# Kernel optimization log

Hardware: AMD Instinct MI355X
Metric: run time of the kernel (lower is better)

The kernel has to match this reference:

```python
import jax, jax.numpy as jnp
import numpy as np

B, S = 2048, 512
INPUT_SIZE, OUTPUT_SIZE = 64, 16
KEY_SIZE, VALUE_SIZE = 64, 64
RECALL_SIZE, MEMORY_SIZE, HIDDEN_SIZE = 2, 3, 32


def setup_inputs() -> dict:
    key = jax.random.key(0)
    ks = jax.random.split(key, 15)
    s = 0.05
    def W(k, o, i):
        return jax.random.normal(k, (o, i), jnp.float32) * s
    def b(k, o):
        return jax.random.normal(k, (o,), jnp.float32) * s
    gru_in = INPUT_SIZE + RECALL_SIZE
    return {
        "inputs": jax.random.normal(ks[0], (B, S, INPUT_SIZE), jnp.float32),
        "w_ih": W(ks[1], 3 * HIDDEN_SIZE, gru_in),
        "w_hh": W(ks[2], 3 * HIDDEN_SIZE, HIDDEN_SIZE),
        "b_ih": b(ks[3], 3 * HIDDEN_SIZE),
        "b_hh": b(ks[4], 3 * HIDDEN_SIZE),
        "W_key": W(ks[5], KEY_SIZE, HIDDEN_SIZE),
        "b_key": b(ks[6], KEY_SIZE),
        "W_query": W(ks[7], KEY_SIZE, HIDDEN_SIZE),
        "b_query": b(ks[8], KEY_SIZE),
        "W_value": W(ks[9], VALUE_SIZE, HIDDEN_SIZE),
        "b_value": b(ks[10], VALUE_SIZE),
        "W_recall": W(ks[11], RECALL_SIZE, VALUE_SIZE),
        "b_recall": b(ks[12], RECALL_SIZE),
        "W_out": W(ks[13], OUTPUT_SIZE, HIDDEN_SIZE),
        "b_out": b(ks[14], OUTPUT_SIZE),
    }


def reference(inputs, w_ih, w_hh, b_ih, b_hh, W_key, b_key, W_query, b_query,
              W_value, b_value, W_recall, b_recall, W_out, b_out):
    Bsz, Slen, _ = inputs.shape
    slot_ids = jnp.arange(MEMORY_SIZE)

    def step(carry, xs):
        h, keys, vals, retr = carry
        xt, t = xs
        # GRUCell (PyTorch gate order r, z, n)
        x = jnp.concatenate([xt, retr], axis=1)
        gx = x @ w_ih.T + b_ih
        gh = h @ w_hh.T + b_hh
        xr, xz, xn = jnp.split(gx, 3, axis=1)
        hr, hz, hn = jnp.split(gh, 3, axis=1)
        r = jax.nn.sigmoid(xr + hr)
        z = jax.nn.sigmoid(xz + hz)
        n = jnp.tanh(xn + r * hn)
        h_new = (1.0 - z) * n + z * h
        # flush hidden state exactly at t == memory_size
        h_new = jnp.where(t == MEMORY_SIZE, 0.0, h_new)
        counter = jnp.minimum(t, MEMORY_SIZE)  # slots written before this step
        # read memory (attention over first `counter` slots)
        q = h_new @ W_query.T + b_query                      # (B, K)
        scores = jnp.einsum('bk,bmk->bm', q, keys)           # (B, M)
        mask = slot_ids < counter
        attn = jax.nn.softmax(jnp.where(mask, scores, -1e30), axis=-1)
        read = jnp.einsum('bm,bmv->bv', attn, vals)          # (B, V)
        retr_new = jnp.where(counter > 0, read @ W_recall.T + b_recall, 0.0)
        # write memory (one-hot scatter into slot t, only while t < memory_size)
        k_w = h_new @ W_key.T + b_key
        v_w = h_new @ W_value.T + b_value
        onehot = (slot_ids == t).astype(keys.dtype)          # all-zero once t >= M
        keys = keys + onehot[None, :, None] * k_w[:, None, :]
        vals = vals + onehot[None, :, None] * v_w[:, None, :]
        out = h_new @ W_out.T + b_out
        return (h_new, keys, vals, retr_new), (out, h_new)

    carry0 = (
        jnp.zeros((Bsz, HIDDEN_SIZE), inputs.dtype),
        jnp.zeros((Bsz, MEMORY_SIZE, KEY_SIZE), inputs.dtype),
        jnp.zeros((Bsz, MEMORY_SIZE, VALUE_SIZE), inputs.dtype),
        jnp.zeros((Bsz, RECALL_SIZE), inputs.dtype),
    )
    xs = (jnp.transpose(inputs, (1, 0, 2)), jnp.arange(Slen))
    _, (outs, hids) = jax.lax.scan(step, carry0, xs)
    outputs = jnp.transpose(outs, (1, 0, 2))                 # (B, S, O)
    hiddens = jax.lax.stop_gradient(jnp.transpose(hids, (1, 0, 2)))  # detached
    return (outputs, hiddens)
```

## Files before the change

kernel.cpp:

```cpp
#include <hip/hip_runtime.h>


typedef __attribute__((ext_vector_type(4))) float f32x4;
typedef __attribute__((ext_vector_type(8))) __bf16 bf16x8;

#define NB 2048
#define SL 512
#define NIN 64
#define NH 32
#define NO 16

__device__ __forceinline__ float rcpf_(float x) { return __builtin_amdgcn_rcpf(x); }
__device__ __forceinline__ float sigmoidf_(float x) {
  return rcpf_(1.0f + __expf(-x));
}
__device__ __forceinline__ float tanhf_(float x) {
  return 1.0f - 2.0f * rcpf_(__expf(2.0f * x) + 1.0f);
}
__device__ __forceinline__ f32x4 splat4(float v) {
  f32x4 r; r[0] = v; r[1] = v; r[2] = v; r[3] = v; return r;
}

template <int CTRL>
__device__ __forceinline__ float dpp_add_(float v) {
  int p = __builtin_amdgcn_update_dpp(0, __float_as_int(v), CTRL, 0xF, 0xF, true);
  return v + __int_as_float(p);
}
__device__ __forceinline__ float rowsum16(float v) {
  v = dpp_add_<0x121>(v);
  v = dpp_add_<0x122>(v);
  v = dpp_add_<0x124>(v);
  v = dpp_add_<0x128>(v);
  return v;
}

__device__ __forceinline__ uint32_t cvtpk_(float lo, float hi) {
  uint32_t r;
  asm("v_cvt_pk_bf16_f32 %0, %1, %2" : "=v"(r) : "v"(lo), "v"(hi));
  return r;
}

__device__ __forceinline__ bf16x8 frag4(uint32_t a, uint32_t b, uint32_t c, uint32_t d) {
  union { uint32_t u[4]; bf16x8 v; } x;
  x.u[0] = a; x.u[1] = b; x.u[2] = c; x.u[3] = d;
  return x.v;
}

__device__ __forceinline__ float pick4v(f32x4 v, int w) {
  float a = (w & 2) ? v[2] : v[0];
  float b = (w & 2) ? v[3] : v[1];
  return (w & 1) ? b : a;
}
__device__ __forceinline__ float pick4f(float a0, float a1, float a2, float a3, int w) {
  float a = (w & 2) ? a2 : a0;
  float b = (w & 2) ? a3 : a1;
  return (w & 1) ? b : a;
}

__device__ __forceinline__ bf16x8 ldfrag(const float* __restrict__ W, int indim,
                                         int row, int k0) {
  bf16x8 r;
#pragma unroll
  for (int j = 0; j < 8; ++j) {
    int k = k0 + j;
    float w = (k < indim) ? W[row * indim + k] : 0.0f;
    r[j] = (__bf16)w;
  }
  return r;
}
__device__ __forceinline__ bf16x8 ldfragS(const float* __restrict__ W, int row, int q4) {
  bf16x8 r;
#pragma unroll
  for (int j = 0; j < 8; ++j) {
    int k = 4 * q4 + (j >> 1) + ((j & 1) ? 16 : 0);
    r[j] = (__bf16)W[row * 32 + k];
  }
  return r;
}
__device__ __forceinline__ bf16x8 ldfragT(const float* __restrict__ W, int ncol,
                                          int col, int k0) {
  bf16x8 r;
#pragma unroll
  for (int j = 0; j < 8; ++j) r[j] = (__bf16)W[(k0 + j) * ncol + col];
  return r;
}

#define MFMA(A, B, C) __builtin_amdgcn_mfma_f32_16x16x32_bf16((A), (B), (C), 0, 0, 0)

__global__ __launch_bounds__(256, 1)
void kvmr_kernel(const float* __restrict__ inputs,
                 const float* __restrict__ w_ih,
                 const float* __restrict__ w_hh,
                 const float* __restrict__ b_ih,
                 const float* __restrict__ b_hh,
                 const float* __restrict__ W_key,
                 const float* __restrict__ b_key,
                 const float* __restrict__ W_query,
                 const float* __restrict__ b_query,
                 const float* __restrict__ W_value,
                 const float* __restrict__ b_value,
                 const float* __restrict__ W_recall,
                 const float* __restrict__ b_recall,
                 const float* __restrict__ W_out,
                 const float* __restrict__ b_out,
                 float* __restrict__ out_all) {
  const int tid = threadIdx.x;
  const int l  = tid & 63;
  const int c  = l & 15;
  const int q4 = l >> 4;
  const int w  = tid >> 6;
  const int b0 = blockIdx.x * 16;

  __shared__ __align__(16) uint32_t h_pk[4][16 * 16];
  __shared__ __align__(16) __bf16 kv_pro[4][3][16 * 64];

  bf16x8 Bih[6][2];
  bf16x8 BhhS[6];
#pragma unroll
  for (int g = 0; g < 6; ++g) {
#pragma unroll
    for (int kc = 0; kc < 2; ++kc)
      Bih[g][kc] = ldfrag(w_ih, 66, 16 * g + c, 32 * kc + 8 * q4);
    BhhS[g] = ldfragS(w_hh, 16 * g + c, q4);
  }
  bf16x8 BqS[4], BkS[4], BvS[4];
#pragma unroll
  for (int g = 0; g < 4; ++g) {
    BqS[g] = ldfragS(W_query, 16 * g + c, q4);
    BkS[g] = ldfragS(W_key,   16 * g + c, q4);
    BvS[g] = ldfragS(W_value, 16 * g + c, q4);
  }
  bf16x8 BoS = ldfragS(W_out, c, q4);

  float wih64[6], wih65[6];
#pragma unroll
  for (int g = 0; g < 6; ++g) {
    wih64[g] = w_ih[(16 * g + c) * 66 + 64];
    wih65[g] = w_ih[(16 * g + c) * 66 + 65];
  }
  float wr0f[4], wr1f[4];
#pragma unroll
  for (int g = 0; g < 4; ++g) {
    wr0f[g] = W_recall[16 * g + c];
    wr1f[g] = W_recall[64 + 16 * g + c];
  }

  float bias_rz[4], bias_xn[2], bias_hn[2];
#pragma unroll
  for (int g = 0; g < 4; ++g) bias_rz[g] = b_ih[16 * g + c] + b_hh[16 * g + c];
#pragma unroll
  for (int gg = 0; gg < 2; ++gg) {
    bias_xn[gg] = b_ih[64 + 16 * gg + c];
    bias_hn[gg] = b_hh[64 + 16 * gg + c];
  }
  float bq4[4], bk4[4], bv4[4];
#pragma unroll
  for (int g = 0; g < 4; ++g) {
    bq4[g] = b_query[16 * g + c];
    bk4[g] = b_key[16 * g + c];
    bv4[g] = b_value[16 * g + c];
  }
  float bo1 = b_out[c];
  float br0 = b_recall[0], br1 = b_recall[1];

  float* outW = out_all + (size_t)(b0 + 4 * q4 + w) * SL * NO + c;
  float* hidW = out_all + (size_t)NB * SL * NO + (size_t)(b0 + 4 * q4 + w) * SL * NH + c;

  f32x4 hD0 = splat4(0.0f), hD1 = splat4(0.0f);
  f32x4 keysR[3][4], valsR[3][4];
#pragma unroll
  for (int s = 0; s < 3; ++s)
#pragma unroll
    for (int g = 0; g < 4; ++g) { keysR[s][g] = splat4(0.0f); valsR[s][g] = splat4(0.0f); }

  f32x4 hPartRZ[4], hPartHN[2];
#pragma unroll
  for (int g = 0; g < 4; ++g) hPartRZ[g] = splat4(bias_rz[g]);
#pragma unroll
  for (int gg = 0; gg < 2; ++gg) hPartHN[gg] = splat4(bias_hn[gg]);
  float retr0c[4] = {0.f, 0.f, 0.f, 0.f};
  float retr1c[4] = {0.f, 0.f, 0.f, 0.f};

  const float* xp = inputs + (size_t)(b0 + c) * (SL * NIN) + 8 * q4;
  f32x4 xb[2][4];
#pragma unroll
  for (int p = 0; p < 2; ++p) {
    const float* xq = xp + p * NIN;
    xb[p][0] = *(const f32x4*)(xq + 0);
    xb[p][1] = *(const f32x4*)(xq + 4);
    xb[p][2] = *(const f32x4*)(xq + 32);
    xb[p][3] = *(const f32x4*)(xq + 36);
  }

#pragma unroll
  for (int t = 0; t < 3; ++t) {
    const int pb = t & 1;
    bf16x8 ax0, ax1;
#pragma unroll
    for (int j = 0; j < 4; ++j) {
      ax0[j]     = (__bf16)xb[pb][0][j];
      ax0[4 + j] = (__bf16)xb[pb][1][j];
      ax1[j]     = (__bf16)xb[pb][2][j];
      ax1[4 + j] = (__bf16)xb[pb][3][j];
    }
    {
      const float* xq = xp + (t + 2) * NIN;
      xb[pb][0] = *(const f32x4*)(xq + 0);
      xb[pb][1] = *(const f32x4*)(xq + 4);
      xb[pb][2] = *(const f32x4*)(xq + 32);
      xb[pb][3] = *(const f32x4*)(xq + 36);
    }

    f32x4 accRZ[4], accXN[2];
#pragma unroll
    for (int g = 0; g < 4; ++g) {
      f32x4 a = hPartRZ[g];
#pragma unroll
      for (int r = 0; r < 4; ++r) a[r] += retr0c[r] * wih64[g] + retr1c[r] * wih65[g];
      a = MFMA(ax0, Bih[g][0], a);
      a = MFMA(ax1, Bih[g][1], a);
      accRZ[g] = a;
    }
#pragma unroll
    for (int gg = 0; gg < 2; ++gg) {
      f32x4 a = splat4(bias_xn[gg]);
#pragma unroll
      for (int r = 0; r < 4; ++r) a[r] += retr0c[r] * wih64[4 + gg] + retr1c[r] * wih65[4 + gg];
      a = MFMA(ax0, Bih[4 + gg][0], a);
      a = MFMA(ax1, Bih[4 + gg][1], a);
      accXN[gg] = a;
    }

    f32x4 hn0, hn1;
#pragma unroll
    for (int r = 0; r < 4; ++r) {
      float rg0 = sigmoidf_(accRZ[0][r]);
      float zg0 = sigmoidf_(accRZ[2][r]);
      float ng0 = tanhf_(accXN[0][r] + rg0 * hPartHN[0][r]);
      hn0[r] = (1.0f - zg0) * ng0 + zg0 * hD0[r];
      float rg1 = sigmoidf_(accRZ[1][r]);
      float zg1 = sigmoidf_(accRZ[3][r]);
      float ng1 = tanhf_(accXN[1][r] + rg1 * hPartHN[1][r]);
      hn1[r] = (1.0f - zg1) * ng1 + zg1 * hD1[r];
    }
    hD0 = hn0; hD1 = hn1;

    hidW[t * NH]      = pick4v(hn0, w);
    hidW[t * NH + 16] = pick4v(hn1, w);
#pragma unroll
    for (int r = 0; r < 4; ++r)
      h_pk[w][(4 * q4 + r) * 16 + c] = cvtpk_(hn0[r], hn1[r]);
    bf16x8 hA = *(const bf16x8*)&h_pk[w][c * 16 + 4 * q4];

#pragma unroll
    for (int g = 0; g < 4; ++g) hPartRZ[g] = MFMA(hA, BhhS[g], splat4(bias_rz[g]));
#pragma unroll
    for (int gg = 0; gg < 2; ++gg) hPartHN[gg] = MFMA(hA, BhhS[4 + gg], splat4(bias_hn[gg]));
    f32x4 oT = MFMA(hA, BoS, splat4(bo1));
    outW[t * NO] = pick4v(oT, w);

    f32x4 qT[4], kT[4], vT[4];
#pragma unroll
    for (int g = 0; g < 4; ++g) {
      qT[g] = MFMA(hA, BqS[g], splat4(bq4[g]));
      kT[g] = MFMA(hA, BkS[g], splat4(bk4[g]));
      vT[g] = MFMA(hA, BvS[g], splat4(bv4[g]));
    }

#pragma unroll
    for (int r = 0; r < 4; ++r) {
      float d0 = qT[0][r] * keysR[0][0][r] + qT[1][r] * keysR[0][1][r] +
                 qT[2][r] * keysR[0][2][r] + qT[3][r] * keysR[0][3][r];
      float d1 = qT[0][r] * keysR[1][0][r] + qT[1][r] * keysR[1][1][r] +
                 qT[2][r] * keysR[1][2][r] + qT[3][r] * keysR[1][3][r];
      float s0 = (t > 0) ? rowsum16(d0) : -1e30f;
      float s1 = (t > 1) ? rowsum16(d1) : -1e30f;
      float s2 = -1e30f;
      float mx = fmaxf(s0, fmaxf(s1, s2));
      float e0 = __expf(s0 - mx), e1 = __expf(s1 - mx), e2 = __expf(s2 - mx);
      float inv = rcpf_(e0 + e1 + e2);
      float u0 = 0.f, u1 = 0.f;
#pragma unroll
      for (int g = 0; g < 4; ++g) {
        float rd = (e0 * valsR[0][g][r] + e1 * valsR[1][g][r] + e2 * valsR[2][g][r]) * inv;
        u0 += rd * wr0f[g];
        u1 += rd * wr1f[g];
      }
      u0 = rowsum16(u0);
      u1 = rowsum16(u1);
      retr0c[r] = (t > 0) ? (u0 + br0) : 0.0f;
      retr1c[r] = (t > 0) ? (u1 + br1) : 0.0f;
    }

#pragma unroll
    for (int g = 0; g < 4; ++g) { keysR[t][g] = kT[g]; valsR[t][g] = vT[g]; }
  }

#pragma unroll
  for (int s = 0; s < 3; ++s)
#pragma unroll
    for (int g = 0; g < 4; ++g)
#pragma unroll
      for (int r = 0; r < 4; ++r)
        kv_pro[w][s][(4 * q4 + r) * 64 + 16 * g + c] = (__bf16)keysR[s][g][r];

  bf16x8 Bwq[2][2];
#pragma unroll
  for (int ch = 0; ch < 2; ++ch)
#pragma unroll
    for (int ct = 0; ct < 2; ++ct)
      Bwq[ch][ct] = ldfragT(W_query, 32, 16 * ct + c, 32 * ch + 8 * q4);

  float M0c[3][4], M1c[3][4], Cq[3][4], VRa[3][4], VRb[3][4];
#pragma unroll
  for (int s = 0; s < 3; ++s) {
    const bf16x8 ak0 = *(const bf16x8*)&kv_pro[w][s][c * 64 + 8 * q4];
    const bf16x8 ak1 = *(const bf16x8*)&kv_pro[w][s][c * 64 + 32 + 8 * q4];
    f32x4 m0 = MFMA(ak1, Bwq[1][0], MFMA(ak0, Bwq[0][0], splat4(0.0f)));
    f32x4 m1 = MFMA(ak1, Bwq[1][1], MFMA(ak0, Bwq[0][1], splat4(0.0f)));
#pragma unroll
    for (int r = 0; r < 4; ++r) {
      M0c[s][r] = m0[r];
      M1c[s][r] = m1[r];
      Cq[s][r] = rowsum16(keysR[s][0][r] * bq4[0] + keysR[s][1][r] * bq4[1] +
                          keysR[s][2][r] * bq4[2] + keysR[s][3][r] * bq4[3]);
      VRa[s][r] = rowsum16(valsR[s][0][r] * wr0f[0] + valsR[s][1][r] * wr0f[1] +
                           valsR[s][2][r] * wr0f[2] + valsR[s][3][r] * wr0f[3]);
      VRb[s][r] = rowsum16(valsR[s][0][r] * wr1f[0] + valsR[s][1][r] * wr1f[1] +
                           valsR[s][2][r] * wr1f[2] + valsR[s][3][r] * wr1f[3]);
    }
  }

  float M0w[3], M1w[3], Cqw[3], VAw[3], VBw[3];
#pragma unroll
  for (int s = 0; s < 3; ++s) {
    M0w[s] = pick4f(M0c[s][0], M0c[s][1], M0c[s][2], M0c[s][3], w);
    M1w[s] = pick4f(M1c[s][0], M1c[s][1], M1c[s][2], M1c[s][3], w);
    Cqw[s] = pick4f(Cq[s][0],  Cq[s][1],  Cq[s][2],  Cq[s][3],  w);
    VAw[s] = pick4f(VRa[s][0], VRa[s][1], VRa[s][2], VRa[s][3], w);
    VBw[s] = pick4f(VRb[s][0], VRb[s][1], VRb[s][2], VRb[s][3], w);
  }

  hidW[3 * NH]      = 0.0f;
  hidW[3 * NH + 16] = 0.0f;
  outW[3 * NO]      = bo1;

  float retr0, retr1;
  {
    float s0 = Cqw[0], s1 = Cqw[1], s2 = Cqw[2];
    float mx = fmaxf(s0, fmaxf(s1, s2));
    float e0 = __expf(s0 - mx), e1 = __expf(s1 - mx), e2 = __expf(s2 - mx);
    float inv = rcpf_(e0 + e1 + e2);
    retr0 = br0 + (e0 * VAw[0] + e1 * VAw[1] + e2 * VAw[2]) * inv;
    retr1 = br1 + (e0 * VBw[0] + e1 * VBw[1] + e2 * VBw[2]) * inv;
  }

  float hprz0 = 0.0f, hprz1 = 0.0f, hprz2 = 0.0f, hprz3 = 0.0f;
  float hphn0 = bias_hn[0], hphn1 = bias_hn[1];
  float h0p = 0.0f, h1p = 0.0f;

  const f32x4 Zq = splat4(0.0f);
  f32x4 biasQ[6];
#pragma unroll
  for (int g = 0; g < 4; ++g) biasQ[g] = splat4(bias_rz[g]);
  biasQ[4] = splat4(bias_xn[0]);
  biasQ[5] = splat4(bias_xn[1]);
  const f32x4 bhnQ0 = splat4(bias_hn[0]);
  const f32x4 bhnQ1 = splat4(bias_hn[1]);
  const f32x4 boQ   = splat4(bo1);

  const int bp0 = 4 * (16 * ((l >> 2) & 3) + 4 * (l >> 4));
  const int bp1 = bp0 + 4;
  const int bp2 = bp0 + 8;
  const int bp3 = bp0 + 12;

  const float* xgp = inputs + (size_t)(b0 + 4 * (c >> 2) + w) * (SL * NIN) +
                     (size_t)(c & 3) * NIN + 8 * q4;
  f32x4 xg[4];
#define LOADXG(T) {                                                           \
    const float* q_ = xgp + (size_t)(T) * NIN;                                \
    xg[0] = *(const f32x4*)(q_ + 0);                                          \
    xg[1] = *(const f32x4*)(q_ + 4);                                          \
    xg[2] = *(const f32x4*)(q_ + 32);                                         \
    xg[3] = *(const f32x4*)(q_ + 36);                                         \
  }
#define XACOMP(DST) {                                                         \
    bf16x8 ax0, ax1;                                                          \
    _Pragma("unroll") for (int j = 0; j < 4; ++j) {                           \
      ax0[j]     = (__bf16)xg[0][j];                                          \
      ax0[4 + j] = (__bf16)xg[1][j];                                          \
      ax1[j]     = (__bf16)xg[2][j];                                          \
      ax1[4 + j] = (__bf16)xg[3][j];                                          \
    }                                                                         \
    _Pragma("unroll") for (int g = 0; g < 6; ++g)                             \
      DST[g] = MFMA(ax1, Bih[g][1], MFMA(ax0, Bih[g][0], biasQ[g]));          \
  }

  f32x4 xaA[6], xaB[6];
  LOADXG(4)
  XACOMP(xaA)
  LOADXG(8)

  float sbh0[16], sbh1[16], sbo[16];

#define STEP(XC, R, U) {                                                      \
    float pr0 = XC[0][R] + hprz0 + retr0 * wih64[0] + retr1 * wih65[0];       \
    float pr1 = XC[1][R] + hprz1 + retr0 * wih64[1] + retr1 * wih65[1];       \
    float pz0 = XC[2][R] + hprz2 + retr0 * wih64[2] + retr1 * wih65[2];       \
    float pz1 = XC[3][R] + hprz3 + retr0 * wih64[3] + retr1 * wih65[3];       \
    float pn0 = XC[4][R] + retr0 * wih64[4] + retr1 * wih65[4];               \
    float pn1 = XC[5][R] + retr0 * wih64[5] + retr1 * wih65[5];               \
    float rg0 = sigmoidf_(pr0), rg1 = sigmoidf_(pr1);                         \
    float zg0 = sigmoidf_(pz0), zg1 = sigmoidf_(pz1);                         \
    float ng0 = tanhf_(pn0 + rg0 * hphn0);                                    \
    float ng1 = tanhf_(pn1 + rg1 * hphn1);                                    \
    float h0 = (1.0f - zg0) * ng0 + zg0 * h0p;                                \
    float h1 = (1.0f - zg1) * ng1 + zg1 * h1p;                                \
    h0p = h0; h1p = h1;                                                       \
    sbh0[U] = h0; sbh1[U] = h1;                                               \
    uint32_t hpk = cvtpk_(h0, h1);                                            \
    uint32_t f0 = (uint32_t)__builtin_amdgcn_ds_bpermute(bp0, (int)hpk);      \
    uint32_t f1 = (uint32_t)__builtin_amdgcn_ds_bpermute(bp1, (int)hpk);      \
    uint32_t f2 = (uint32_t)__builtin_amdgcn_ds_bpermute(bp2, (int)hpk);      \
    uint32_t f3 = (uint32_t)__builtin_amdgcn_ds_bpermute(bp3, (int)hpk);      \
    bf16x8 hA = frag4(f0, f1, f2, f3);                                        \
    { f32x4 d_;                                                               \
      d_ = MFMA(hA, BhhS[0], Zq);    hprz0 = d_[0];                           \
      d_ = MFMA(hA, BhhS[1], Zq);    hprz1 = d_[0];                           \
      d_ = MFMA(hA, BhhS[2], Zq);    hprz2 = d_[0];                           \
      d_ = MFMA(hA, BhhS[3], Zq);    hprz3 = d_[0];                           \
      d_ = MFMA(hA, BhhS[4], bhnQ0); hphn0 = d_[0];                           \
      d_ = MFMA(hA, BhhS[5], bhnQ1); hphn1 = d_[0];                           \
      d_ = MFMA(hA, BoS,     boQ);   sbo[U] = d_[0];                          \
    }                                                                         \
    float p0 = h0 * M0w[0] + h1 * M1w[0];                                     \
    float p1 = h0 * M0w[1] + h1 * M1w[1];                                     \
    float p2 = h0 * M0w[2] + h1 * M1w[2];                                     \
    p0 = rowsum16(p0) + Cqw[0];                                               \
    p1 = rowsum16(p1) + Cqw[1];                                               \
    p2 = rowsum16(p2) + Cqw[2];                                               \
    float mx = fmaxf(p0, fmaxf(p1, p2));                                      \
    float e0 = __expf(p0 - mx), e1 = __expf(p1 - mx), e2 = __expf(p2 - mx);   \
    float inv = rcpf_(e0 + e1 + e2);                                          \
    retr0 = br0 + (e0 * VAw[0] + e1 * VAw[1] + e2 * VAw[2]) * inv;            \
    retr1 = br1 + (e0 * VBw[0] + e1 * VBw[1] + e2 * VBw[2]) * inv;            \
  }

#define GROUP4(TT, XC, XN, U0, DONEXT, DOPF) {                                \
    if (DONEXT) { XACOMP(XN) }                                                \
    if (DOPF)   { LOADXG((TT) + 8) }                                          \
    STEP(XC, 0, (U0) + 0)                                                     \
    STEP(XC, 1, (U0) + 1)                                                     \
    STEP(XC, 2, (U0) + 2)                                                     \
    STEP(XC, 3, (U0) + 3)                                                     \
  }

#define FLUSH(TB, N)                                                          \
    _Pragma("unroll") for (int r = 0; r < (N); ++r) {                         \
      hidW[((TB) + r) * NH]      = sbh0[r];                                   \
      hidW[((TB) + r) * NH + 16] = sbh1[r];                                   \
      outW[((TB) + r) * NO]      = sbo[r];                                    \
    }

  for (int tb = 4; tb < 500; tb += 16) {
    GROUP4(tb + 0,  xaA, xaB, 0,  1, 1)
    GROUP4(tb + 4,  xaB, xaA, 4,  1, 1)
    GROUP4(tb + 8,  xaA, xaB, 8,  1, 1)
    GROUP4(tb + 12, xaB, xaA, 12, 1, 1)
    FLUSH(tb, 16)
  }
  {
    GROUP4(500, xaA, xaB, 0, 1, 1)
    GROUP4(504, xaB, xaA, 4, 1, 0)
    GROUP4(508, xaA, xaB, 8, 0, 0)
    FLUSH(500, 12)
  }
#undef STEP
#undef GROUP4
#undef FLUSH
#undef LOADXG
#undef XACOMP
}

extern "C" void kernel_launch(void* const* d_in, const int* in_sizes, int n_in,
                              void* d_out, int out_size, void* d_ws, size_t ws_size,
                              hipStream_t stream) {
  (void)in_sizes; (void)n_in; (void)out_size; (void)d_ws; (void)ws_size;
  const float* inputs   = (const float*)d_in[0];
  const float* w_ih     = (const float*)d_in[1];
  const float* w_hh     = (const float*)d_in[2];
  const float* b_ih     = (const float*)d_in[3];
  const float* b_hh     = (const float*)d_in[4];
  const float* W_key    = (const float*)d_in[5];
  const float* b_key    = (const float*)d_in[6];
  const float* W_query  = (const float*)d_in[7];
  const float* b_query  = (const float*)d_in[8];
  const float* W_value  = (const float*)d_in[9];
  const float* b_value  = (const float*)d_in[10];
  const float* W_recall = (const float*)d_in[11];
  const float* b_recall = (const float*)d_in[12];
  const float* W_out    = (const float*)d_in[13];
  const float* b_out    = (const float*)d_in[14];
  float* out = (float*)d_out;

  kvmr_kernel<<<dim3(128), dim3(256), 0, stream>>>(
      inputs, w_ih, w_hh, b_ih, b_hh, W_key, b_key, W_query, b_query,
      W_value, b_value, W_recall, b_recall, W_out, b_out, out);
}
```

Baseline: 602.7 us.

## Run two independent batch recurrences per wave with half the threads per block

Each block now launches 2 waves instead of 4, and each wave interleaves the steady-state recurrence for two batch rows (A and B). The aim is to hide the serial dependency latency of one chain (MFMA, bpermute, transcendentals) behind the other. The retrieval-to-gate contribution is also folded algebraically: softmax weights times precomputed value·w_ih products, with the recall bias moved into the gate bias. Outputs are written every step rather than staged and flushed in blocks of 16. The trade-off is higher register pressure, and the prologue steps still index shared buffers by w while only two waves exist.

After: 746.9 us. 1.24x slower.

```diff
diff --git a/kernel.cpp b/kernel.cpp
--- a/kernel.cpp
+++ b/kernel.cpp
@@ -46,15 +46,15 @@
   return x.v;
 }
 
-__device__ __forceinline__ float pick4v(f32x4 v, int w) {
-  float a = (w & 2) ? v[2] : v[0];
-  float b = (w & 2) ? v[3] : v[1];
-  return (w & 1) ? b : a;
-}
-__device__ __forceinline__ float pick4f(float a0, float a1, float a2, float a3, int w) {
-  float a = (w & 2) ? a2 : a0;
-  float b = (w & 2) ? a3 : a1;
-  return (w & 1) ? b : a;
+__device__ __forceinline__ float pick4v(f32x4 v, int ww) {
+  float a = (ww & 2) ? v[2] : v[0];
+  float b = (ww & 2) ? v[3] : v[1];
+  return (ww & 1) ? b : a;
+}
+__device__ __forceinline__ float pick4f(float a0, float a1, float a2, float a3, int ww) {
+  float a = (ww & 2) ? a2 : a0;
+  float b = (ww & 2) ? a3 : a1;
+  return (ww & 1) ? b : a;
 }
 
 __device__ __forceinline__ bf16x8 ldfrag(const float* __restrict__ W, int indim,
@@ -87,7 +87,7 @@
 
 #define MFMA(A, B, C) __builtin_amdgcn_mfma_f32_16x16x32_bf16((A), (B), (C), 0, 0, 0)
 
-__global__ __launch_bounds__(256, 1)
+__global__ __launch_bounds__(128, 1)
 void kvmr_kernel(const float* __restrict__ inputs,
                  const float* __restrict__ w_ih,
                  const float* __restrict__ w_hh,
@@ -109,10 +109,12 @@
   const int c  = l & 15;
   const int q4 = l >> 4;
   const int w  = tid >> 6;
+  const int wA = w;
+  const int wB = w + 2;
   const int b0 = blockIdx.x * 16;
 
-  __shared__ __align__(16) uint32_t h_pk[4][16 * 16];
-  __shared__ __align__(16) __bf16 kv_pro[4][3][16 * 64];
+  __shared__ __align__(16) uint32_t h_pk[2][16 * 16];
+  __shared__ __align__(16) __bf16 kv_pro[2][3][16 * 64];
 
   bf16x8 Bih[6][2];
   bf16x8 BhhS[6];
@@ -163,8 +165,10 @@
   float bo1 = b_out[c];
   float br0 = b_recall[0], br1 = b_recall[1];
 
-  float* outW = out_all + (size_t)(b0 + 4 * q4 + w) * SL * NO + c;
-  float* hidW = out_all + (size_t)NB * SL * NO + (size_t)(b0 + 4 * q4 + w) * SL * NH + c;
+  float* outWA = out_all + (size_t)(b0 + 4 * q4 + wA) * SL * NO + c;
+  float* hidWA = out_all + (size_t)NB * SL * NO + (size_t)(b0 + 4 * q4 + wA) * SL * NH + c;
+  float* outWB = out_all + (size_t)(b0 + 4 * q4 + wB) * SL * NO + c;
+  float* hidWB = out_all + (size_t)NB * SL * NO + (size_t)(b0 + 4 * q4 + wB) * SL * NH + c;
 
   f32x4 hD0 = splat4(0.0f), hD1 = splat4(0.0f);
   f32x4 keysR[3][4], valsR[3][4];
@@ -245,8 +249,10 @@
     }
     hD0 = hn0; hD1 = hn1;
 
-    hidW[t * NH]      = pick4v(hn0, w);
-    hidW[t * NH + 16] = pick4v(hn1, w);
+    hidWA[t * NH]      = pick4v(hn0, wA);
+    hidWA[t * NH + 16] = pick4v(hn1, wA);
+    hidWB[t * NH]      = pick4v(hn0, wB);
+    hidWB[t * NH + 16] = pick4v(hn1, wB);
 #pragma unroll
     for (int r = 0; r < 4; ++r)
       h_pk[w][(4 * q4 + r) * 16 + c] = cvtpk_(hn0[r], hn1[r]);
@@ -257,7 +263,8 @@
 #pragma unroll
     for (int gg = 0; gg < 2; ++gg) hPartHN[gg] = MFMA(hA, BhhS[4 + gg], splat4(bias_hn[gg]));
     f32x4 oT = MFMA(hA, BoS, splat4(bo1));
-    outW[t * NO] = pick4v(oT, w);
+    outWA[t * NO] = pick4v(oT, wA);
+    outWB[t * NO] = pick4v(oT, wB);
 
     f32x4 qT[4], kT[4], vT[4];
 #pragma unroll
@@ -331,155 +338,238 @@
     }
   }
 
-  float M0w[3], M1w[3], Cqw[3], VAw[3], VBw[3];
+  float Ma0[3], Ma1[3], Cqa[3], VAa[3], VBa[3];
+  float Mb0[3], Mb1[3], Cqb[3], VAb[3], VBb[3];
 #pragma unroll
   for (int s = 0; s < 3; ++s) {
-    M0w[s] = pick4f(M0c[s][0], M0c[s][1], M0c[s][2], M0c[s][3], w);
-    M1w[s] = pick4f(M1c[s][0], M1c[s][1], M1c[s][2], M1c[s][3], w);
-    Cqw[s] = pick4f(Cq[s][0],  Cq[s][1],  Cq[s][2],  Cq[s][3],  w);
-    VAw[s] = pick4f(VRa[s][0], VRa[s][1], VRa[s][2], VRa[s][3], w);
-    VBw[s] = pick4f(VRb[s][0], VRb[s][1], VRb[s][2], VRb[s][3], w);
-  }
-
-  hidW[3 * NH]      = 0.0f;
-  hidW[3 * NH + 16] = 0.0f;
-  outW[3 * NO]      = bo1;
-
-  float retr0, retr1;
-  {
-    float s0 = Cqw[0], s1 = Cqw[1], s2 = Cqw[2];
-    float mx = fmaxf(s0, fmaxf(s1, s2));
-    float e0 = __expf(s0 - mx), e1 = __expf(s1 - mx), e2 = __expf(s2 - mx);
-    float inv = rcpf_(e0 + e1 + e2);
-    retr0 = br0 + (e0 * VAw[0] + e1 * VAw[1] + e2 * VAw[2]) * inv;
-    retr1 = br1 + (e0 * VBw[0] + e1 * VBw[1] + e2 * VBw[2]) * inv;
-  }
-
-  float hprz0 = 0.0f, hprz1 = 0.0f, hprz2 = 0.0f, hprz3 = 0.0f;
-  float hphn0 = bias_hn[0], hphn1 = bias_hn[1];
-  float h0p = 0.0f, h1p = 0.0f;
+    Ma0[s] = pick4f(M0c[s][0], M0c[s][1], M0c[s][2], M0c[s][3], wA);
+    Ma1[s] = pick4f(M1c[s][0], M1c[s][1], M1c[s][2], M1c[s][3], wA);
+    Cqa[s] = pick4f(Cq[s][0],  Cq[s][1],  Cq[s][2],  Cq[s][3],  wA);
+    VAa[s] = pick4f(VRa[s][0], VRa[s][1], VRa[s][2], VRa[s][3], wA);
+    VBa[s] = pick4f(VRb[s][0], VRb[s][1], VRb[s][2], VRb[s][3], wA);
+    Mb0[s] = pick4f(M0c[s][0], M0c[s][1], M0c[s][2], M0c[s][3], wB);
+    Mb1[s] = pick4f(M1c[s][0], M1c[s][1], M1c[s][2], M1c[s][3], wB);
+    Cqb[s] = pick4f(Cq[s][0],  Cq[s][1],  Cq[s][2],  Cq[s][3],  wB);
+    VAb[s] = pick4f(VRa[s][0], VRa[s][1], VRa[s][2], VRa[s][3], wB);
+    VBb[s] = pick4f(VRb[s][0], VRb[s][1], VRb[s][2], VRb[s][3], wB);
+  }
+
+  float GVa[3][6], GVb[3][6], brc[6];
+#pragma unroll
+  for (int g = 0; g < 6; ++g) {
+    brc[g] = br0 * wih64[g] + br1 * wih65[g];
+#pragma unroll
+    for (int s = 0; s < 3; ++s) {
+      GVa[s][g] = VAa[s] * wih64[g] + VBa[s] * wih65[g];
+      GVb[s][g] = VAb[s] * wih64[g] + VBb[s] * wih65[g];
+    }
+  }
 
   const f32x4 Zq = splat4(0.0f);
   f32x4 biasQ[6];
 #pragma unroll
-  for (int g = 0; g < 4; ++g) biasQ[g] = splat4(bias_rz[g]);
-  biasQ[4] = splat4(bias_xn[0]);
-  biasQ[5] = splat4(bias_xn[1]);
+  for (int g = 0; g < 4; ++g) biasQ[g] = splat4(bias_rz[g] + brc[g]);
+  biasQ[4] = splat4(bias_xn[0] + brc[4]);
+  biasQ[5] = splat4(bias_xn[1] + brc[5]);
   const f32x4 bhnQ0 = splat4(bias_hn[0]);
   const f32x4 bhnQ1 = splat4(bias_hn[1]);
   const f32x4 boQ   = splat4(bo1);
+
+  hidWA[3 * NH] = 0.0f; hidWA[3 * NH + 16] = 0.0f; outWA[3 * NO] = bo1;
+  hidWB[3 * NH] = 0.0f; hidWB[3 * NH + 16] = 0.0f; outWB[3 * NO] = bo1;
+
+  float aa0, aa1, aa2, ab0, ab1, ab2;
+  {
+    float e0 = __expf(Cqa[0]), e1 = __expf(Cqa[1]), e2 = __expf(Cqa[2]);
+    float inv = rcpf_(e0 + e1 + e2);
+    aa0 = e0 * inv; aa1 = e1 * inv; aa2 = e2 * inv;
+  }
+  {
+    float e0 = __expf(Cqb[0]), e1 = __expf(Cqb[1]), e2 = __expf(Cqb[2]);
+    float inv = rcpf_(e0 + e1 + e2);
+    ab0 = e0 * inv; ab1 = e1 * inv; ab2 = e2 * inv;
+  }
+
+  float hprzA0 = 0.f, hprzA1 = 0.f, hprzA2 = 0.f, hprzA3 = 0.f;
+  float hphnA0 = bias_hn[0], hphnA1 = bias_hn[1];
+  float hA0p = 0.f, hA1p = 0.f;
+  float hprzB0 = 0.f, hprzB1 = 0.f, hprzB2 = 0.f, hprzB3 = 0.f;
+  float hphnB0 = bias_hn[0], hphnB1 = bias_hn[1];
+  float hB0p = 0.f, hB1p = 0.f;
 
   const int bp0 = 4 * (16 * ((l >> 2) & 3) + 4 * (l >> 4));
   const int bp1 = bp0 + 4;
   const int bp2 = bp0 + 8;
   const int bp3 = bp0 + 12;
 
-  const float* xgp = inputs + (size_t)(b0 + 4 * (c >> 2) + w) * (SL * NIN) +
-                     (size_t)(c & 3) * NIN + 8 * q4;
-  f32x4 xg[4];
-#define LOADXG(T) {                                                           \
-    const float* q_ = xgp + (size_t)(T) * NIN;                                \
-    xg[0] = *(const f32x4*)(q_ + 0);                                          \
-    xg[1] = *(const f32x4*)(q_ + 4);                                          \
-    xg[2] = *(const f32x4*)(q_ + 32);                                         \
-    xg[3] = *(const f32x4*)(q_ + 36);                                         \
-  }
-#define XACOMP(DST) {                                                         \
+  const float* xgpA = inputs + (size_t)(b0 + 4 * (c >> 2) + wA) * (SL * NIN) +
+                      (size_t)(c & 3) * NIN + 8 * q4;
+  const float* xgpB = inputs + (size_t)(b0 + 4 * (c >> 2) + wB) * (SL * NIN) +
+                      (size_t)(c & 3) * NIN + 8 * q4;
+  f32x4 xgA[4], xgB[4];
+#define LOADXGA(T) {                                                          \
+    const float* q_ = xgpA + (size_t)(T) * NIN;                               \
+    xgA[0] = *(const f32x4*)(q_ + 0);                                         \
+    xgA[1] = *(const f32x4*)(q_ + 4);                                         \
+    xgA[2] = *(const f32x4*)(q_ + 32);                                        \
+    xgA[3] = *(const f32x4*)(q_ + 36);                                        \
+  }
+#define LOADXGB(T) {                                                          \
+    const float* q_ = xgpB + (size_t)(T) * NIN;                               \
+    xgB[0] = *(const f32x4*)(q_ + 0);                                         \
+    xgB[1] = *(const f32x4*)(q_ + 4);                                         \
+    xgB[2] = *(const f32x4*)(q_ + 32);                                        \
+    xgB[3] = *(const f32x4*)(q_ + 36);                                        \
+  }
+#define XACOMPA(DST) {                                                        \
     bf16x8 ax0, ax1;                                                          \
     _Pragma("unroll") for (int j = 0; j < 4; ++j) {                           \
-      ax0[j]     = (__bf16)xg[0][j];                                          \
-      ax0[4 + j] = (__bf16)xg[1][j];                                          \
-      ax1[j]     = (__bf16)xg[2][j];                                          \
-      ax1[4 + j] = (__bf16)xg[3][j];                                          \
+      ax0[j]     = (__bf16)xgA[0][j];                                         \
+      ax0[4 + j] = (__bf16)xgA[1][j];                                         \
+      ax1[j]     = (__bf16)xgA[2][j];                                         \
+      ax1[4 + j] = (__bf16)xgA[3][j];                                         \
     }                                                                         \
     _Pragma("unroll") for (int g = 0; g < 6; ++g)                             \
       DST[g] = MFMA(ax1, Bih[g][1], MFMA(ax0, Bih[g][0], biasQ[g]));          \
   }
-
-  f32x4 xaA[6], xaB[6];
-  LOADXG(4)
-  XACOMP(xaA)
-  LOADXG(8)
-
-  float sbh0[16], sbh1[16], sbo[16];
-
-#define STEP(XC, R, U) {                                                      \
-    float pr0 = XC[0][R] + hprz0 + retr0 * wih64[0] + retr1 * wih65[0];       \
-    float pr1 = XC[1][R] + hprz1 + retr0 * wih64[1] + retr1 * wih65[1];       \
-    float pz0 = XC[2][R] + hprz2 + retr0 * wih64[2] + retr1 * wih65[2];       \
-    float pz1 = XC[3][R] + hprz3 + retr0 * wih64[3] + retr1 * wih65[3];       \
-    float pn0 = XC[4][R] + retr0 * wih64[4] + retr1 * wih65[4];               \
-    float pn1 = XC[5][R] + retr0 * wih64[5] + retr1 * wih65[5];               \
-    float rg0 = sigmoidf_(pr0), rg1 = sigmoidf_(pr1);                         \
-    float zg0 = sigmoidf_(pz0), zg1 = sigmoidf_(pz1);                         \
-    float ng0 = tanhf_(pn0 + rg0 * hphn0);                                    \
-    float ng1 = tanhf_(pn1 + rg1 * hphn1);                                    \
-    float h0 = (1.0f - zg0) * ng0 + zg0 * h0p;                                \
-    float h1 = (1.0f - zg1) * ng1 + zg1 * h1p;                                \
-    h0p = h0; h1p = h1;                                                       \
-    sbh0[U] = h0; sbh1[U] = h1;                                               \
-    uint32_t hpk = cvtpk_(h0, h1);                                            \
-    uint32_t f0 = (uint32_t)__builtin_amdgcn_ds_bpermute(bp0, (int)hpk);      \
-    uint32_t f1 = (uint32_t)__builtin_amdgcn_ds_bpermute(bp1, (int)hpk);      \
-    uint32_t f2 = (uint32_t)__builtin_amdgcn_ds_bpermute(bp2, (int)hpk);      \
-    uint32_t f3 = (uint32_t)__builtin_amdgcn_ds_bpermute(bp3, (int)hpk);      \
-    bf16x8 hA = frag4(f0, f1, f2, f3);                                        \
+#define XACOMPB(DST) {                                                        \
+    bf16x8 ax0, ax1;                                                          \
+    _Pragma("unroll") for (int j = 0; j < 4; ++j) {                           \
+      ax0[j]     = (__bf16)xgB[0][j];                                         \
+      ax0[4 + j] = (__bf16)xgB[1][j];                                         \
+      ax1[j]     = (__bf16)xgB[2][j];                                         \
+      ax1[4 + j] = (__bf16)xgB[3][j];                                         \
+    }                                                                         \
+    _Pragma("unroll") for (int g = 0; g < 6; ++g)                             \
+      DST[g] = MFMA(ax1, Bih[g][1], MFMA(ax0, Bih[g][0], biasQ[g]));          \
+  }
+
+  f32x4 xaA0[6], xaA1[6], xaB0[6], xaB1[6];
+  LOADXGA(4) LOADXGB(4)
+  XACOMPA(xaA0) XACOMPB(xaB0)
+  LOADXGA(8) LOADXGB(8)
+
+#define STEP2(XA, XB, R, T) {                                                 \
+                                                                 \
+    float rtA0 = aa0 * GVa[0][0] + aa1 * GVa[1][0] + aa2 * GVa[2][0];         \
+    float rtA1 = aa0 * GVa[0][1] + aa1 * GVa[1][1] + aa2 * GVa[2][1];         \
+    float rtA2 = aa0 * GVa[0][2] + aa1 * GVa[1][2] + aa2 * GVa[2][2];         \
+    float rtA3 = aa0 * GVa[0][3] + aa1 * GVa[1][3] + aa2 * GVa[2][3];         \
+    float rtA4 = aa0 * GVa[0][4] + aa1 * GVa[1][4] + aa2 * GVa[2][4];         \
+    float rtA5 = aa0 * GVa[0][5] + aa1 * GVa[1][5] + aa2 * GVa[2][5];         \
+    float rgA0 = sigmoidf_(XA[0][R] + hprzA0 + rtA0);                         \
+    float rgA1 = sigmoidf_(XA[1][R] + hprzA1 + rtA1);                         \
+    float zgA0 = sigmoidf_(XA[2][R] + hprzA2 + rtA2);                         \
+    float zgA1 = sigmoidf_(XA[3][R] + hprzA3 + rtA3);                         \
+    float ngA0 = tanhf_(XA[4][R] + rtA4 + rgA0 * hphnA0);                     \
+    float ngA1 = tanhf_(XA[5][R] + rtA5 + rgA1 * hphnA1);                     \
+    float hA0 = (1.0f - zgA0) * ngA0 + zgA0 * hA0p;                           \
+    float hA1 = (1.0f - zgA1) * ngA1 + zgA1 * hA1p;                           \
+    hA0p = hA0; hA1p = hA1;                                                   \
+                                                                 \
+    float rtB0 = ab0 * GVb[0][0] + ab1 * GVb[1][0] + ab2 * GVb[2][0];         \
+    float rtB1 = ab0 * GVb[0][1] + ab1 * GVb[1][1] + ab2 * GVb[2][1];         \
+    float rtB2 = ab0 * GVb[0][2] + ab1 * GVb[1][2] + ab2 * GVb[2][2];         \
+    float rtB3 = ab0 * GVb[0][3] + ab1 * GVb[1][3] + ab2 * GVb[2][3];         \
+    float rtB4 = ab0 * GVb[0][4] + ab1 * GVb[1][4] + ab2 * GVb[2][4];         \
+    float rtB5 = ab0 * GVb[0][5] + ab1 * GVb[1][5] + ab2 * GVb[2][5];         \
+    float rgB0 = sigmoidf_(XB[0][R] + hprzB0 + rtB0);                         \
+    float rgB1 = sigmoidf_(XB[1][R] + hprzB1 + rtB1);                         \
+    float zgB0 = sigmoidf_(XB[2][R] + hprzB2 + rtB2);                         \
+    float zgB1 = sigmoidf_(XB[3][R] + hprzB3 + rtB3);                         \
+    float ngB0 = tanhf_(XB[4][R] + rtB4 + rgB0 * hphnB0);                     \
+    float ngB1 = tanhf_(XB[5][R] + rtB5 + rgB1 * hphnB1);                     \
+    float hB0 = (1.0f - zgB0) * ngB0 + zgB0 * hB0p;                           \
+    float hB1 = (1.0f - zgB1) * ngB1 + zgB1 * hB1p;                           \
+    hB0p = hB0; hB1p = hB1;                                                   \
+                 \
+    uint32_t hpkA = cvtpk_(hA0, hA1);                                         \
+    uint32_t hpkB = cvtpk_(hB0, hB1);                                         \
+    uint32_t fA0 = (uint32_t)__builtin_amdgcn_ds_bpermute(bp0, (int)hpkA);    \
+    uint32_t fA1 = (uint32_t)__builtin_amdgcn_ds_bpermute(bp1, (int)hpkA);    \
+    uint32_t fA2 = (uint32_t)__builtin_amdgcn_ds_bpermute(bp2, (int)hpkA);    \
+    uint32_t fA3 = (uint32_t)__builtin_amdgcn_ds_bpermute(bp3, (int)hpkA);    \
+    uint32_t fB0 = (uint32_t)__builtin_amdgcn_ds_bpermute(bp0, (int)hpkB);    \
+    uint32_t fB1 = (uint32_t)__builtin_amdgcn_ds_bpermute(bp1, (int)hpkB);    \
+    uint32_t fB2 = (uint32_t)__builtin_amdgcn_ds_bpermute(bp2, (int)hpkB);    \
+    uint32_t fB3 = (uint32_t)__builtin_amdgcn_ds_bpermute(bp3, (int)hpkB);    \
+    bf16x8 hAf = frag4(fA0, fA1, fA2, fA3);                                   \
+    float oA;                                                                 \
     { f32x4 d_;                                                               \
-      d_ = MFMA(hA, BhhS[0], Zq);    hprz0 = d_[0];                           \
-      d_ = MFMA(hA, BhhS[1], Zq);    hprz1 = d_[0];                           \
-      d_ = MFMA(hA, BhhS[2], Zq);    hprz2 = d_[0];                           \
-      d_ = MFMA(hA, BhhS[3], Zq);    hprz3 = d_[0];                           \
-      d_ = MFMA(hA, BhhS[4], bhnQ0); hphn0 = d_[0];                           \
-      d_ = MFMA(hA, BhhS[5], bhnQ1); hphn1 = d_[0];                           \
-      d_ = MFMA(hA, BoS,     boQ);   sbo[U] = d_[0];                          \
+      d_ = MFMA(hAf, BhhS[0], Zq);    hprzA0 = d_[0];                         \
+      d_ = MFMA(hAf, BhhS[1], Zq);    hprzA1 = d_[0];                         \
+      d_ = MFMA(hAf, BhhS[2], Zq);    hprzA2 = d_[0];                         \
+      d_ = MFMA(hAf, BhhS[3], Zq);    hprzA3 = d_[0];                         \
+      d_ = MFMA(hAf, BhhS[4], bhnQ0); hphnA0 = d_[0];                         \
+      d_ = MFMA(hAf, BhhS[5], bhnQ1); hphnA1 = d_[0];                         \
+      d_ = MFMA(hAf, BoS,     boQ);   oA = d_[0];                             \
     }                                                                         \
-    float p0 = h0 * M0w[0] + h1 * M1w[0];                                     \
-    float p1 = h0 * M0w[1] + h1 * M1w[1];                                     \
-    float p2 = h0 * M0w[2] + h1 * M1w[2];                                     \
-    p0 = rowsum16(p0) + Cqw[0];                                               \
-    p1 = rowsum16(p1) + Cqw[1];                                               \
-    p2 = rowsum16(p2) + Cqw[2];                                               \
-    float mx = fmaxf(p0, fmaxf(p1, p2));                                      \
-    float e0 = __expf(p0 - mx), e1 = __expf(p1 - mx), e2 = __expf(p2 - mx);   \
-    float inv = rcpf_(e0 + e1 + e2);                                          \
-    retr0 = br0 + (e0 * VAw[0] + e1 * VAw[1] + e2 * VAw[2]) * inv;            \
-    retr1 = br1 + (e0 * VBw[0] + e1 * VBw[1] + e2 * VBw[2]) * inv;            \
-  }
-
-#define GROUP4(TT, XC, XN, U0, DONEXT, DOPF) {                                \
-    if (DONEXT) { XACOMP(XN) }                                                \
-    if (DOPF)   { LOADXG((TT) + 8) }                                          \
-    STEP(XC, 0, (U0) + 0)                                                     \
-    STEP(XC, 1, (U0) + 1)                                                     \
-    STEP(XC, 2, (U0) + 2)                                                     \
-    STEP(XC, 3, (U0) + 3)                                                     \
-  }
-
-#define FLUSH(TB, N)                                                          \
-    _Pragma("unroll") for (int r = 0; r < (N); ++r) {                         \
-      hidW[((TB) + r) * NH]      = sbh0[r];                                   \
-      hidW[((TB) + r) * NH + 16] = sbh1[r];                                   \
-      outW[((TB) + r) * NO]      = sbo[r];                                    \
-    }
+    bf16x8 hBf = frag4(fB0, fB1, fB2, fB3);                                   \
+    float oB;                                                                 \
+    { f32x4 d_;                                                               \
+      d_ = MFMA(hBf, BhhS[0], Zq);    hprzB0 = d_[0];                         \
+      d_ = MFMA(hBf, BhhS[1], Zq);    hprzB1 = d_[0];                         \
+      d_ = MFMA(hBf, BhhS[2], Zq);    hprzB2 = d_[0];                         \
+      d_ = MFMA(hBf, BhhS[3], Zq);    hprzB3 = d_[0];                         \
+      d_ = MFMA(hBf, BhhS[4], bhnQ0); hphnB0 = d_[0];                         \
+      d_ = MFMA(hBf, BhhS[5], bhnQ1); hphnB1 = d_[0];                         \
+      d_ = MFMA(hBf, BoS,     boQ);   oB = d_[0];                             \
+    }                                                                         \
+    \
+    float paA0 = hA0 * Ma0[0] + hA1 * Ma1[0];                                 \
+    float paA1 = hA0 * Ma0[1] + hA1 * Ma1[1];                                 \
+    float paA2 = hA0 * Ma0[2] + hA1 * Ma1[2];                                 \
+    paA0 = rowsum16(paA0) + Cqa[0];                                           \
+    paA1 = rowsum16(paA1) + Cqa[1];                                           \
+    paA2 = rowsum16(paA2) + Cqa[2];                                           \
+    float eA0 = __expf(paA0), eA1 = __expf(paA1), eA2 = __expf(paA2);         \
+    float invA = rcpf_(eA0 + eA1 + eA2);                                      \
+    aa0 = eA0 * invA; aa1 = eA1 * invA; aa2 = eA2 * invA;                     \
+                                                             \
+    float paB0 = hB0 * Mb0[0] + hB1 * Mb1[0];                                 \
+    float paB1 = hB0 * Mb0[1] + hB1 * Mb1[1];                                 \
+    float paB2 = hB0 * Mb0[2] + hB1 * Mb1[2];                                 \
+    paB0 = rowsum16(paB0) + Cqb[0];                                           \
+    paB1 = rowsum16(paB1) + Cqb[1];                                           \
+    paB2 = rowsum16(paB2) + Cqb[2];                                           \
+    float eB0 = __expf(paB0), eB1 = __expf(paB1), eB2 = __expf(paB2);         \
+    float invB = rcpf_(eB0 + eB1 + eB2);                                      \
+    ab0 = eB0 * invB; ab1 = eB1 * invB; ab2 = eB2 * invB;                     \
+                                         \
+    hidWA[(T) * NH]      = hA0;                                               \
+    hidWA[(T) * NH + 16] = hA1;                                               \
+    outWA[(T) * NO]      = oA;                                                \
+    hidWB[(T) * NH]      = hB0;                                               \
+    hidWB[(T) * NH + 16] = hB1;                                               \
+    outWB[(T) * NO]      = oB;                                                \
+  }
+
+#define GROUP2(TT, XAc, XAn, XBc, XBn, DONEXT, DOPF) {                        \
+    if (DONEXT) { XACOMPA(XAn) XACOMPB(XBn) }                                 \
+    if (DOPF)   { LOADXGA((TT) + 8) LOADXGB((TT) + 8) }                       \
+    STEP2(XAc, XBc, 0, (TT) + 0)                                              \
+    STEP2(XAc, XBc, 1, (TT) + 1)                                              \
+    STEP2(XAc, XBc, 2, (TT) + 2)                                              \
+    STEP2(XAc, XBc, 3, (TT) + 3)                                              \
+  }
 
   for (int tb = 4; tb < 500; tb += 16) {
-    GROUP4(tb + 0,  xaA, xaB, 0,  1, 1)
-    GROUP4(tb + 4,  xaB, xaA, 4,  1, 1)
-    GROUP4(tb + 8,  xaA, xaB, 8,  1, 1)
-    GROUP4(tb + 12, xaB, xaA, 12, 1, 1)
-    FLUSH(tb, 16)
+    GROUP2(tb + 0,  xaA0, xaA1, xaB0, xaB1, 1, 1)
+    GROUP2(tb + 4,  xaA1, xaA0, xaB1, xaB0, 1, 1)
+    GROUP2(tb + 8,  xaA0, xaA1, xaB0, xaB1, 1, 1)
+    GROUP2(tb + 12, xaA1, xaA0, xaB1, xaB0, 1, 1)
   }
   {
-    GROUP4(500, xaA, xaB, 0, 1, 1)
-    GROUP4(504, xaB, xaA, 4, 1, 0)
-    GROUP4(508, xaA, xaB, 8, 0, 0)
-    FLUSH(500, 12)
-  }
-#undef STEP
-#undef GROUP4
-#undef FLUSH
-#undef LOADXG
-#undef XACOMP
+    GROUP2(500, xaA0, xaA1, xaB0, xaB1, 1, 1)
+    GROUP2(504, xaA1, xaA0, xaB1, xaB0, 1, 0)
+    GROUP2(508, xaA0, xaA1, xaB0, xaB1, 0, 0)
+  }
+#undef STEP2
+#undef GROUP2
+#undef LOADXGA
+#undef LOADXGB
+#undef XACOMPA
+#undef XACOMPB
 }
 
 extern "C" void kernel_launch(void* const* d_in, const int* in_sizes, int n_in,
@@ -503,7 +593,7 @@
   const float* b_out    = (const float*)d_in[14];
   float* out = (float*)d_out;
 
-  kvmr_kernel<<<dim3(128), dim3(256), 0, stream>>>(
+  kvmr_kernel<<<dim3(128), dim3(128), 0, stream>>>(
       inputs, w_ih, w_hh, b_ih, b_hh, W_key, b_key, W_query, b_query,
       W_value, b_value, W_recall, b_recall, W_out, b_out, out);
 }
```

## Fold recall projection into gate weights and drop softmax max-subtraction

Applied to the files above, without the earlier changes.

Precomputes the product of the value-recall projection with the recall input columns of w_ih, so each step computes gate contributions directly from the attention weights. The recall bias contribution is folded into the MFMA bias vectors. The softmax drops its max-subtraction, which risks overflow if scores grow large. The attention computation moves ahead of the MFMAs to shorten the serial dependency chain. Per-step global stores replace the buffered 16-step flush, which cuts register pressure but issues scattered stores inside the recurrent loop.

New measurement: 574.4 us. 1.05x faster.

```diff
diff --git a/kernel.cpp b/kernel.cpp
--- a/kernel.cpp
+++ b/kernel.cpp
@@ -341,33 +341,39 @@
     VBw[s] = pick4f(VRb[s][0], VRb[s][1], VRb[s][2], VRb[s][3], w);
   }
 
+  float GVw[3][6], brc[6];
+#pragma unroll
+  for (int g = 0; g < 6; ++g) {
+    brc[g] = br0 * wih64[g] + br1 * wih65[g];
+#pragma unroll
+    for (int s = 0; s < 3; ++s)
+      GVw[s][g] = VAw[s] * wih64[g] + VBw[s] * wih65[g];
+  }
+
+  const f32x4 Zq = splat4(0.0f);
+  f32x4 biasQ[6];
+#pragma unroll
+  for (int g = 0; g < 4; ++g) biasQ[g] = splat4(bias_rz[g] + brc[g]);
+  biasQ[4] = splat4(bias_xn[0] + brc[4]);
+  biasQ[5] = splat4(bias_xn[1] + brc[5]);
+  const f32x4 bhnQ0 = splat4(bias_hn[0]);
+  const f32x4 bhnQ1 = splat4(bias_hn[1]);
+  const f32x4 boQ   = splat4(bo1);
+
   hidW[3 * NH]      = 0.0f;
   hidW[3 * NH + 16] = 0.0f;
   outW[3 * NO]      = bo1;
 
-  float retr0, retr1;
+  float a0, a1, a2;
   {
-    float s0 = Cqw[0], s1 = Cqw[1], s2 = Cqw[2];
-    float mx = fmaxf(s0, fmaxf(s1, s2));
-    float e0 = __expf(s0 - mx), e1 = __expf(s1 - mx), e2 = __expf(s2 - mx);
+    float e0 = __expf(Cqw[0]), e1 = __expf(Cqw[1]), e2 = __expf(Cqw[2]);
     float inv = rcpf_(e0 + e1 + e2);
-    retr0 = br0 + (e0 * VAw[0] + e1 * VAw[1] + e2 * VAw[2]) * inv;
-    retr1 = br1 + (e0 * VBw[0] + e1 * VBw[1] + e2 * VBw[2]) * inv;
+    a0 = e0 * inv; a1 = e1 * inv; a2 = e2 * inv;
   }
 
   float hprz0 = 0.0f, hprz1 = 0.0f, hprz2 = 0.0f, hprz3 = 0.0f;
   float hphn0 = bias_hn[0], hphn1 = bias_hn[1];
   float h0p = 0.0f, h1p = 0.0f;
-
-  const f32x4 Zq = splat4(0.0f);
-  f32x4 biasQ[6];
-#pragma unroll
-  for (int g = 0; g < 4; ++g) biasQ[g] = splat4(bias_rz[g]);
-  biasQ[4] = splat4(bias_xn[0]);
-  biasQ[5] = splat4(bias_xn[1]);
-  const f32x4 bhnQ0 = splat4(bias_hn[0]);
-  const f32x4 bhnQ1 = splat4(bias_hn[1]);
-  const f32x4 boQ   = splat4(bo1);
 
   const int bp0 = 4 * (16 * ((l >> 2) & 3) + 4 * (l >> 4));
   const int bp1 = bp0 + 4;
@@ -401,29 +407,39 @@
   XACOMP(xaA)
   LOADXG(8)
 
-  float sbh0[16], sbh1[16], sbo[16];
-
-#define STEP(XC, R, U) {                                                      \
-    float pr0 = XC[0][R] + hprz0 + retr0 * wih64[0] + retr1 * wih65[0];       \
-    float pr1 = XC[1][R] + hprz1 + retr0 * wih64[1] + retr1 * wih65[1];       \
-    float pz0 = XC[2][R] + hprz2 + retr0 * wih64[2] + retr1 * wih65[2];       \
-    float pz1 = XC[3][R] + hprz3 + retr0 * wih64[3] + retr1 * wih65[3];       \
-    float pn0 = XC[4][R] + retr0 * wih64[4] + retr1 * wih65[4];               \
-    float pn1 = XC[5][R] + retr0 * wih64[5] + retr1 * wih65[5];               \
-    float rg0 = sigmoidf_(pr0), rg1 = sigmoidf_(pr1);                         \
-    float zg0 = sigmoidf_(pz0), zg1 = sigmoidf_(pz1);                         \
-    float ng0 = tanhf_(pn0 + rg0 * hphn0);                                    \
-    float ng1 = tanhf_(pn1 + rg1 * hphn1);                                    \
+#define STEP(XC, R, T) {                                                      \
+    float rt0 = a0 * GVw[0][0] + a1 * GVw[1][0] + a2 * GVw[2][0];             \
+    float rt1 = a0 * GVw[0][1] + a1 * GVw[1][1] + a2 * GVw[2][1];             \
+    float rt2 = a0 * GVw[0][2] + a1 * GVw[1][2] + a2 * GVw[2][2];             \
+    float rt3 = a0 * GVw[0][3] + a1 * GVw[1][3] + a2 * GVw[2][3];             \
+    float rt4 = a0 * GVw[0][4] + a1 * GVw[1][4] + a2 * GVw[2][4];             \
+    float rt5 = a0 * GVw[0][5] + a1 * GVw[1][5] + a2 * GVw[2][5];             \
+    float rg0 = sigmoidf_(XC[0][R] + hprz0 + rt0);                            \
+    float rg1 = sigmoidf_(XC[1][R] + hprz1 + rt1);                            \
+    float zg0 = sigmoidf_(XC[2][R] + hprz2 + rt2);                            \
+    float zg1 = sigmoidf_(XC[3][R] + hprz3 + rt3);                            \
+    float ng0 = tanhf_(XC[4][R] + rt4 + rg0 * hphn0);                         \
+    float ng1 = tanhf_(XC[5][R] + rt5 + rg1 * hphn1);                         \
     float h0 = (1.0f - zg0) * ng0 + zg0 * h0p;                                \
     float h1 = (1.0f - zg1) * ng1 + zg1 * h1p;                                \
     h0p = h0; h1p = h1;                                                       \
-    sbh0[U] = h0; sbh1[U] = h1;                                               \
     uint32_t hpk = cvtpk_(h0, h1);                                            \
     uint32_t f0 = (uint32_t)__builtin_amdgcn_ds_bpermute(bp0, (int)hpk);      \
     uint32_t f1 = (uint32_t)__builtin_amdgcn_ds_bpermute(bp1, (int)hpk);      \
     uint32_t f2 = (uint32_t)__builtin_amdgcn_ds_bpermute(bp2, (int)hpk);      \
     uint32_t f3 = (uint32_t)__builtin_amdgcn_ds_bpermute(bp3, (int)hpk);      \
+              \
+    float p0 = h0 * M0w[0] + h1 * M1w[0];                                     \
+    float p1 = h0 * M0w[1] + h1 * M1w[1];                                     \
+    float p2 = h0 * M0w[2] + h1 * M1w[2];                                     \
+    p0 = rowsum16(p0) + Cqw[0];                                               \
+    p1 = rowsum16(p1) + Cqw[1];                                               \
+    p2 = rowsum16(p2) + Cqw[2];                                               \
+    float e0 = __expf(p0), e1 = __expf(p1), e2 = __expf(p2);                  \
+    float inv = rcpf_(e0 + e1 + e2);                                          \
+    a0 = e0 * inv; a1 = e1 * inv; a2 = e2 * inv;                              \
     bf16x8 hA = frag4(f0, f1, f2, f3);                                        \
+    float oo;                                                                 \
     { f32x4 d_;                                                               \
       d_ = MFMA(hA, BhhS[0], Zq);    hprz0 = d_[0];                           \
       d_ = MFMA(hA, BhhS[1], Zq);    hprz1 = d_[0];                           \
@@ -431,53 +447,35 @@
       d_ = MFMA(hA, BhhS[3], Zq);    hprz3 = d_[0];                           \
       d_ = MFMA(hA, BhhS[4], bhnQ0); hphn0 = d_[0];                           \
       d_ = MFMA(hA, BhhS[5], bhnQ1); hphn1 = d_[0];                           \
-      d_ = MFMA(hA, BoS,     boQ);   sbo[U] = d_[0];                          \
+      d_ = MFMA(hA, BoS,     boQ);   oo = d_[0];                              \
     }                                                                         \
-    float p0 = h0 * M0w[0] + h1 * M1w[0];                                     \
-    float p1 = h0 * M0w[1] + h1 * M1w[1];                                     \
-    float p2 = h0 * M0w[2] + h1 * M1w[2];                                     \
-    p0 = rowsum16(p0) + Cqw[0];                                               \
-    p1 = rowsum16(p1) + Cqw[1];                                               \
-    p2 = rowsum16(p2) + Cqw[2];                                               \
-    float mx = fmaxf(p0, fmaxf(p1, p2));                                      \
-    float e0 = __expf(p0 - mx), e1 = __expf(p1 - mx), e2 = __expf(p2 - mx);   \
-    float inv = rcpf_(e0 + e1 + e2);                                          \
-    retr0 = br0 + (e0 * VAw[0] + e1 * VAw[1] + e2 * VAw[2]) * inv;            \
-    retr1 = br1 + (e0 * VBw[0] + e1 * VBw[1] + e2 * VBw[2]) * inv;            \
-  }
-
-#define GROUP4(TT, XC, XN, U0, DONEXT, DOPF) {                                \
+    hidW[(T) * NH]      = h0;                                                 \
+    hidW[(T) * NH + 16] = h1;                                                 \
+    outW[(T) * NO]      = oo;                                                 \
+  }
+
+#define GROUP4(TT, XC, XN, DONEXT, DOPF) {                                    \
     if (DONEXT) { XACOMP(XN) }                                                \
     if (DOPF)   { LOADXG((TT) + 8) }                                          \
-    STEP(XC, 0, (U0) + 0)                                                     \
-    STEP(XC, 1, (U0) + 1)                                                     \
-    STEP(XC, 2, (U0) + 2)                                                     \
-    STEP(XC, 3, (U0) + 3)                                                     \
-  }
-
-#define FLUSH(TB, N)                                                          \
-    _Pragma("unroll") for (int r = 0; r < (N); ++r) {                         \
-      hidW[((TB) + r) * NH]      = sbh0[r];                                   \
-      hidW[((TB) + r) * NH + 16] = sbh1[r];                                   \
-      outW[((TB) + r) * NO]      = sbo[r];                                    \
-    }
+    STEP(XC, 0, (TT) + 0)                                                     \
+    STEP(XC, 1, (TT) + 1)                                                     \
+    STEP(XC, 2, (TT) + 2)                                                     \
+    STEP(XC, 3, (TT) + 3)                                                     \
+  }
 
   for (int tb = 4; tb < 500; tb += 16) {
-    GROUP4(tb + 0,  xaA, xaB, 0,  1, 1)
-    GROUP4(tb + 4,  xaB, xaA, 4,  1, 1)
-    GROUP4(tb + 8,  xaA, xaB, 8,  1, 1)
-    GROUP4(tb + 12, xaB, xaA, 12, 1, 1)
-    FLUSH(tb, 16)
+    GROUP4(tb + 0,  xaA, xaB, 1, 1)
+    GROUP4(tb + 4,  xaB, xaA, 1, 1)
+    GROUP4(tb + 8,  xaA, xaB, 1, 1)
+    GROUP4(tb + 12, xaB, xaA, 1, 1)
   }
   {
-    GROUP4(500, xaA, xaB, 0, 1, 1)
-    GROUP4(504, xaB, xaA, 4, 1, 0)
-    GROUP4(508, xaA, xaB, 8, 0, 0)
-    FLUSH(500, 12)
+    GROUP4(500, xaA, xaB, 1, 1)
+    GROUP4(504, xaB, xaA, 1, 0)
+    GROUP4(508, xaA, xaB, 0, 0)
   }
 #undef STEP
 #undef GROUP4
-#undef FLUSH
 #undef LOADXG
 #undef XACOMP
 }
```
